# Performance work log

Hardware: AMD Instinct MI355X
Metric: run time of the kernel (lower is better)

## Reference

```python
import jax, jax.numpy as jnp
import numpy as np

CROP = 512
GRID = 8
NBINS = 256
CLIP_LIMIT = 0.8


def _clahe(x):
    # x: [B, C, H, W] in [0, 1], H and W divisible by GRID
    B, C, H, W = x.shape
    th, tw = H // GRID, W // GRID
    tp = th * tw  # pixels per tile
    # bin index of each pixel (256 uniform bins over [0, 1])
    bins = jnp.clip((x * NBINS).astype(jnp.int32), 0, NBINS - 1)
    # per-tile histograms: [B*C*GRID*GRID, tp] -> scatter-add into 256 bins
    tiles = bins.reshape(B, C, GRID, th, GRID, tw).transpose(0, 1, 2, 4, 3, 5).reshape(-1, tp)
    hist = jax.vmap(lambda b: jnp.zeros((NBINS,), jnp.float32).at[b].add(1.0))(tiles)
    # clip histogram and redistribute excess uniformly
    clip_val = max(CLIP_LIMIT * tp / NBINS, 1.0)
    clipped = jnp.minimum(hist, clip_val)
    excess = (hist - clipped).sum(-1, keepdims=True)
    hist = clipped + excess / NBINS
    # CDF -> LUT per tile, values in [0, 255]
    lut = jnp.clip(jnp.cumsum(hist, -1) * ((NBINS - 1.0) / tp), 0.0, NBINS - 1.0)
    luts = lut.reshape(B, C, GRID, GRID, NBINS)
    # bilinear interpolation between the 4 nearest tile LUTs
    ty = (jnp.arange(H, dtype=jnp.float32) + 0.5) / th - 0.5
    tx = (jnp.arange(W, dtype=jnp.float32) + 0.5) / tw - 0.5
    y0f, x0f = jnp.floor(ty), jnp.floor(tx)
    fy = (ty - y0f)[None, None, :, None]
    fx = (tx - x0f)[None, None, None, :]
    y0 = jnp.clip(y0f, 0, GRID - 1).astype(jnp.int32)
    y1 = jnp.clip(y0f + 1, 0, GRID - 1).astype(jnp.int32)
    x0 = jnp.clip(x0f, 0, GRID - 1).astype(jnp.int32)
    x1 = jnp.clip(x0f + 1, 0, GRID - 1).astype(jnp.int32)
    bi = jnp.arange(B)[:, None, None, None]
    ci = jnp.arange(C)[None, :, None, None]
    Y0 = y0[None, None, :, None]
    Y1 = y1[None, None, :, None]
    X0 = x0[None, None, None, :]
    X1 = x1[None, None, None, :]
    v00 = luts[bi, ci, Y0, X0, bins]
    v01 = luts[bi, ci, Y0, X1, bins]
    v10 = luts[bi, ci, Y1, X0, bins]
    v11 = luts[bi, ci, Y1, X1, bins]
    top = (1.0 - fx) * v00 + fx * v01
    bot = (1.0 - fx) * v10 + fx * v11
    return ((1.0 - fy) * top + fy * bot) / (NBINS - 1.0)


def _augment(x, hflip, vflip, offy, offx, apply_clahe):
    # per-sample horizontal / vertical flips
    x = jnp.where(hflip[:, None, None, None].astype(bool), x[..., ::-1], x)
    x = jnp.where(vflip[:, None, None, None].astype(bool), x[..., ::-1, :], x)
    # per-sample random 512x512 crop
    C = x.shape[1]
    crop = jax.vmap(
        lambda img, oy, ox: jax.lax.dynamic_slice(img, (0, oy, ox), (C, CROP, CROP))
    )(x, offy, offx)
    # RandomApply(CLAHE): compute for all samples, select per sample
    eq = _clahe(crop)
    return jnp.where(apply_clahe[:, None, None, None].astype(bool), eq, crop)


def setup_inputs() -> dict:
    key = jax.random.key(0)
    ks = jax.random.split(key, 6)
    B, C, H, W = 64, 1, 640, 640
    x = jax.random.uniform(ks[0], (B, C, H, W), dtype=jnp.float32)
    hflip = jax.random.randint(ks[1], (B,), 0, 2, dtype=jnp.int32)
    vflip = jax.random.randint(ks[2], (B,), 0, 2, dtype=jnp.int32)
    offy = jax.random.randint(ks[3], (B,), 0, H - CROP + 1, dtype=jnp.int32)
    offx = jax.random.randint(ks[4], (B,), 0, W - CROP + 1, dtype=jnp.int32)
    apply_clahe = jax.random.randint(ks[5], (B,), 0, 2, dtype=jnp.int32)
    return {"x": x, "hflip": hflip, "vflip": vflip, "offy": offy, "offx": offx, "apply_clahe": apply_clahe}


def reference(x, hflip, vflip, offy, offx, apply_clahe):
    return _augment(x, hflip, vflip, offy, offx, apply_clahe)
```

## Files before the change

kernel.cpp:

```cpp
#include <hip/hip_runtime.h>

#define IH 640
#define IW 640
#define CROPSZ 512
#define NGRID 8
#define TILE 64
#define NBINS 256
#define TP (TILE*TILE)
#define CLIPV 12.8f

typedef float fvec4 __attribute__((ext_vector_type(4)));

__global__ __launch_bounds__(256) void clahe_lut_kernel(
    const float* __restrict__ x,
    const int* __restrict__ hflip, const int* __restrict__ vflip,
    const int* __restrict__ offy,  const int* __restrict__ offx,
    const int* __restrict__ apply,
    float* __restrict__ luts)
{
    const int bt = blockIdx.x;
    const int b  = bt >> 6;
    if (!apply[b]) return;
    const int tile = bt & 63;
    const int tyi = tile >> 3, txi = tile & 7;

    const int oy = offy[b], ox = offx[b];
    const int by = tyi * TILE, bx = txi * TILE;
    const int sy = vflip[b] ? (IH - TILE - oy - by) : (oy + by);
    const int sx = hflip[b] ? (IW - TILE - ox - bx) : (ox + bx);

    __shared__ unsigned int hist[4][NBINS];
    const int t    = threadIdx.x;
    const int lane = t & 63;
    const int wid  = t >> 6;
    #pragma unroll
    for (int w = 0; w < 4; ++w) hist[w][t] = 0u;
    __syncthreads();

    const float* __restrict__ xb = x + (size_t)b * (IH * IW);

    #pragma unroll
    for (int k = 0; k < 4; ++k) {
        const int q    = t + k * 256;
        const int row  = q >> 4;
        const int col4 = (q & 15) << 2;
        const fvec4 v = *reinterpret_cast<const fvec4*>(
                             xb + (size_t)(sy + row) * IW + sx + col4);
        #pragma unroll
        for (int j = 0; j < 4; ++j) {
            int bin = (int)(v[j] * 256.0f);
            bin = bin < 0 ? 0 : (bin > 255 ? 255 : bin);
            atomicAdd(&hist[wid][bin], 1u);
        }
    }
    __syncthreads();

    const float h = (float)(hist[0][t] + hist[1][t] + hist[2][t] + hist[3][t]);
    const float clipped = fminf(h, CLIPV);
    float ex = h - clipped;

    #pragma unroll
    for (int off = 32; off > 0; off >>= 1) ex += __shfl_down(ex, off, 64);
    __shared__ float wsum[4];
    if (lane == 0) wsum[wid] = ex;
    __syncthreads();
    const float excess = wsum[0] + wsum[1] + wsum[2] + wsum[3];

    const float hv = clipped + excess * (1.0f / (float)NBINS);

    float s = hv;
    #pragma unroll
    for (int off = 1; off < 64; off <<= 1) {
        const float n = __shfl_up(s, off, 64);
        if (lane >= off) s += n;
    }
    __shared__ float wtot[4];
    if (lane == 63) wtot[wid] = s;
    __syncthreads();
    float prefix = 0.0f;
    for (int w = 0; w < wid; ++w) prefix += wtot[w];
    s += prefix;

    float lut = s * (255.0f / (float)TP);
    lut = fminf(fmaxf(lut, 0.0f), 255.0f);
    luts[(size_t)bt * NBINS + t] = lut;
}

__global__ __launch_bounds__(256) void augment_out_kernel(
    const float* __restrict__ x,
    const int* __restrict__ hflip, const int* __restrict__ vflip,
    const int* __restrict__ offy,  const int* __restrict__ offx,
    const int* __restrict__ apply,
    const float* __restrict__ luts,
    float* __restrict__ out)
{
    const int bid = blockIdx.x;
    const int b   = bid >> 8;
    const int t   = threadIdx.x;
    const int q   = ((bid & 255) << 8) + t;
    const int y   = q >> 7;
    const int x4  = (q & 127) << 2;

    const int hf = hflip[b], vf = vflip[b];
    const int oy = offy[b],  ox = offx[b];
    const int ap = apply[b];

    const int iy = vf ? (IH - 1 - oy - y) : (oy + y);
    const float* __restrict__ row = x + (size_t)b * (IH * IW) + (size_t)iy * IW;

    fvec4 v;
    if (hf) {
        const fvec4 r = *reinterpret_cast<const fvec4*>(row + (IW - 4 - ox - x4));
        v = (fvec4){r.w, r.z, r.y, r.x};
    } else {
        v = *reinterpret_cast<const fvec4*>(row + ox + x4);
    }

    fvec4 o;
    if (ap) {
        const float tyf = (y + 0.5f) * (1.0f / TILE) - 0.5f;
        const float y0f = floorf(tyf);
        const float fy  = tyf - y0f;
        const int   y0  = max(0, min(NGRID - 1, (int)y0f));
        const int   y1  = max(0, min(NGRID - 1, (int)y0f + 1));
        const float* __restrict__ lb = luts + (size_t)b * (64 * NBINS);

        #pragma unroll
        for (int j = 0; j < 4; ++j) {
            const int xx = x4 + j;
            const float txf = (xx + 0.5f) * (1.0f / TILE) - 0.5f;
            const float x0f = floorf(txf);
            const float fx  = txf - x0f;
            const int   x0  = max(0, min(NGRID - 1, (int)x0f));
            const int   x1  = max(0, min(NGRID - 1, (int)x0f + 1));

            int bin = (int)(v[j] * 256.0f);
            bin = bin < 0 ? 0 : (bin > 255 ? 255 : bin);

            const float v00 = lb[((y0 << 3) + x0) * NBINS + bin];
            const float v01 = lb[((y0 << 3) + x1) * NBINS + bin];
            const float v10 = lb[((y1 << 3) + x0) * NBINS + bin];
            const float v11 = lb[((y1 << 3) + x1) * NBINS + bin];

            const float top = (1.0f - fx) * v00 + fx * v01;
            const float bot = (1.0f - fx) * v10 + fx * v11;
            o[j] = ((1.0f - fy) * top + fy * bot) * (1.0f / 255.0f);
        }
    } else {
        o = v;
    }
    __builtin_nontemporal_store(o, reinterpret_cast<fvec4*>(out) + ((size_t)bid * 256 + t));
}

extern "C" void kernel_launch(void* const* d_in, const int* in_sizes, int n_in,
                              void* d_out, int out_size, void* d_ws, size_t ws_size,
                              hipStream_t stream) {
    const float* x     = (const float*)d_in[0];
    const int*   hflip = (const int*)d_in[1];
    const int*   vflip = (const int*)d_in[2];
    const int*   offy  = (const int*)d_in[3];
    const int*   offx  = (const int*)d_in[4];
    const int*   apply = (const int*)d_in[5];
    float*       out   = (float*)d_out;
    float*       luts  = (float*)d_ws;

    hipLaunchKernelGGL(clahe_lut_kernel, dim3(64 * 64), dim3(256), 0, stream,
                       x, hflip, vflip, offy, offx, apply, luts);

    const int nblocks = 64 * (CROPSZ * CROPSZ / 4) / 256;
    hipLaunchKernelGGL(augment_out_kernel, dim3(nblocks), dim3(256), 0, stream,
                       x, hflip, vflip, offy, offx, apply, luts, out);
}
```

Measured before the change: 193.7 us.

## Tile output blocks as 16x64 patches and stage the four neighbour LUTs in shared memory

```diff
diff --git a/kernel.cpp b/kernel.cpp
--- a/kernel.cpp
+++ b/kernel.cpp
@@ -96,10 +96,16 @@
 {
     const int bid = blockIdx.x;
     const int b   = bid >> 8;
-    const int t   = threadIdx.x;
-    const int q   = ((bid & 255) << 8) + t;
-    const int y   = q >> 7;
-    const int x4  = (q & 127) << 2;
+    const int blk = bid & 255;
+    const int cb  = blk & 7;
+    const int rb  = blk >> 3;
+
+    const int t  = threadIdx.x;
+    const int tc = t & 15;
+    const int r  = t >> 4;
+
+    const int y   = rb * 16 + r;
+    const int col = cb * 64 + tc * 4;
 
     const int hf = hflip[b], vf = vflip[b];
     const int oy = offy[b],  ox = offx[b];
@@ -110,46 +116,53 @@
 
     fvec4 v;
     if (hf) {
-        const fvec4 r = *reinterpret_cast<const fvec4*>(row + (IW - 4 - ox - x4));
-        v = (fvec4){r.w, r.z, r.y, r.x};
+        const fvec4 rr = *reinterpret_cast<const fvec4*>(row + (IW - 4 - ox - col));
+        v = (fvec4){rr.w, rr.z, rr.y, rr.x};
     } else {
-        v = *reinterpret_cast<const fvec4*>(row + ox + x4);
+        v = *reinterpret_cast<const fvec4*>(row + ox + col);
     }
 
     fvec4 o;
     if (ap) {
-        const float tyf = (y + 0.5f) * (1.0f / TILE) - 0.5f;
-        const float y0f = floorf(tyf);
-        const float fy  = tyf - y0f;
-        const int   y0  = max(0, min(NGRID - 1, (int)y0f));
-        const int   y1  = max(0, min(NGRID - 1, (int)y0f + 1));
+        const int y0f = (int)floorf((rb * 16 + 0.5f) * (1.0f / TILE) - 0.5f);
+        const int y0  = max(0, min(NGRID - 1, y0f));
+        const int y1  = max(0, min(NGRID - 1, y0f + 1));
+
+        __shared__ fvec4 lutq[2][NBINS];
         const float* __restrict__ lb = luts + (size_t)b * (64 * NBINS);
+        #pragma unroll
+        for (int h = 0; h < 2; ++h) {
+            const int xl = max(0, min(NGRID - 1, cb - 1 + h));
+            const int xr = max(0, min(NGRID - 1, cb + h));
+            fvec4 q;
+            q.x = lb[((y0 << 3) + xl) * NBINS + t];
+            q.y = lb[((y0 << 3) + xr) * NBINS + t];
+            q.z = lb[((y1 << 3) + xl) * NBINS + t];
+            q.w = lb[((y1 << 3) + xr) * NBINS + t];
+            lutq[h][t] = q;
+        }
+        __syncthreads();
+
+        const float fy = (y + 0.5f) * (1.0f / TILE) - 0.5f - (float)y0f;
+        const int   h  = tc >> 3;
+        const float x0ff = (float)(cb - 1 + h);
 
         #pragma unroll
         for (int j = 0; j < 4; ++j) {
-            const int xx = x4 + j;
-            const float txf = (xx + 0.5f) * (1.0f / TILE) - 0.5f;
-            const float x0f = floorf(txf);
-            const float fx  = txf - x0f;
-            const int   x0  = max(0, min(NGRID - 1, (int)x0f));
-            const int   x1  = max(0, min(NGRID - 1, (int)x0f + 1));
-
+            const float fx = (col + j + 0.5f) * (1.0f / TILE) - 0.5f - x0ff;
             int bin = (int)(v[j] * 256.0f);
             bin = bin < 0 ? 0 : (bin > 255 ? 255 : bin);
-
-            const float v00 = lb[((y0 << 3) + x0) * NBINS + bin];
-            const float v01 = lb[((y0 << 3) + x1) * NBINS + bin];
-            const float v10 = lb[((y1 << 3) + x0) * NBINS + bin];
-            const float v11 = lb[((y1 << 3) + x1) * NBINS + bin];
-
-            const float top = (1.0f - fx) * v00 + fx * v01;
-            const float bot = (1.0f - fx) * v10 + fx * v11;
+            const fvec4 q = lutq[h][bin];
+            const float top = (1.0f - fx) * q.x + fx * q.y;
+            const float bot = (1.0f - fx) * q.z + fx * q.w;
             o[j] = ((1.0f - fy) * top + fy * bot) * (1.0f / 255.0f);
         }
     } else {
         o = v;
     }
-    __builtin_nontemporal_store(o, reinterpret_cast<fvec4*>(out) + ((size_t)bid * 256 + t));
+
+    const size_t oidx = (size_t)b * (CROPSZ * CROPSZ / 4) + (size_t)y * (CROPSZ / 4) + (col >> 2);
+    __builtin_nontemporal_store(o, reinterpret_cast<fvec4*>(out) + oidx);
 }
 
 extern "C" void kernel_launch(void* const* d_in, const int* in_sizes, int n_in,
@@ -167,7 +180,6 @@
     hipLaunchKernelGGL(clahe_lut_kernel, dim3(64 * 64), dim3(256), 0, stream,
                        x, hflip, vflip, offy, offx, apply, luts);
 
-    const int nblocks = 64 * (CROPSZ * CROPSZ / 4) / 256;
-    hipLaunchKernelGGL(augment_out_kernel, dim3(nblocks), dim3(256), 0, stream,
+    hipLaunchKernelGGL(augment_out_kernel, dim3(64 * 256), dim3(256), 0, stream,
                        x, hflip, vflip, offy, offx, apply, luts, out);
 }
```

Result: faster. 181.4 us (-6.4%).
